# Performance work log

Measured on AMD Instinct MI355X. Metric: run time of the kernel, lower is better.

## Reference

```python
import jax, jax.numpy as jnp
import numpy as np

N, E = 10000, 160000
F_IN, H1, C1, C2 = 256, 8, 128, 128
SLOPE = 0.2  # PyG GATConv default negative_slope


def setup_inputs() -> dict:
    key = jax.random.key(0)
    ks = jax.random.split(key, 9)
    s = 0.05
    return {
        "x": jax.random.normal(ks[0], (N, F_IN), jnp.float32),
        "edge_index": jax.random.randint(ks[1], (2, E), 0, N),
        "W1": jax.random.normal(ks[2], (F_IN, H1 * C1), jnp.float32) * s,
        "a_src1": jax.random.normal(ks[3], (H1, C1), jnp.float32) * s,
        "a_dst1": jax.random.normal(ks[4], (H1, C1), jnp.float32) * s,
        "b1": jnp.zeros((H1 * C1,), jnp.float32),
        "W2": jax.random.normal(ks[5], (H1 * C1, C2), jnp.float32) * s,
        "a_src2": jax.random.normal(ks[6], (1, C2), jnp.float32) * s,
        "a_dst2": jax.random.normal(ks[7], (1, C2), jnp.float32) * s,
        "b2": jnp.zeros((C2,), jnp.float32),
    }


def gat_conv(x, src, dst, W, a_s, a_d, b, heads, out_ch, concat):
    n = x.shape[0]
    h = (x @ W).reshape(n, heads, out_ch)            # [N,H,C]
    s_src = jnp.einsum("nhc,hc->nh", h, a_s)         # [N,H]
    s_dst = jnp.einsum("nhc,hc->nh", h, a_d)
    e = jax.nn.leaky_relu(s_src[src] + s_dst[dst], SLOPE)   # [Etot,H]
    # segment softmax over incoming edges per destination (self-loops guarantee non-empty segments)
    m = jax.lax.stop_gradient(jax.ops.segment_max(e, dst, num_segments=n))
    p = jnp.exp(e - m[dst])
    denom = jax.ops.segment_sum(p, dst, num_segments=n)
    alpha = p / denom[dst]                            # [Etot,H]
    out = jax.ops.segment_sum(h[src] * alpha[:, :, None], dst, num_segments=n)  # [N,H,C]
    out = out.reshape(n, heads * out_ch) if concat else out.mean(axis=1)
    return out + b


def reference(x, edge_index, W1, a_src1, a_dst1, b1, W2, a_src2, a_dst2, b2):
    n = x.shape[0]
    loops = jnp.arange(n, dtype=edge_index.dtype)     # PyG add_self_loops=True
    src = jnp.concatenate([edge_index[0], loops])
    dst = jnp.concatenate([edge_index[1], loops])
    # dropout layers are identity at inference (training=False)
    h1 = jax.nn.elu(gat_conv(x, src, dst, W1, a_src1, a_dst1, b1, H1, C1, True))
    return gat_conv(h1, src, dst, W2, a_src2, a_dst2, b2, 1, C2, False)
```

## Files before the change

### kernel.cpp

```cpp
#include <hip/hip_runtime.h>
#include <math.h>

#define F_IN 256
#define H1 8
#define C1 128
#define HC1 1024
#define C2 128
#define SLOPE 0.2f

typedef unsigned short u16;
typedef __attribute__((ext_vector_type(8))) short bf16x8;
typedef __attribute__((ext_vector_type(4))) float f32x4;


__device__ __forceinline__ float lrelu(float v) { return v > 0.f ? v : SLOPE * v; }

__device__ __forceinline__ unsigned bf16_rne(float x) {
    unsigned u = __float_as_uint(x);
    u += 0x7fffu + ((u >> 16) & 1u);
    return u >> 16;
}

__device__ __forceinline__ void split2(float a, float b, unsigned& hi, unsigned& lo) {
    unsigned ha = bf16_rne(a), hb = bf16_rne(b);
    float fa = __uint_as_float(ha << 16), fb = __uint_as_float(hb << 16);
    hi = ha | (hb << 16);
    lo = bf16_rne(a - fa) | (bf16_rne(b - fb) << 16);
}

__device__ __forceinline__ void gload16(const u16* g, u16* l) {
    __builtin_amdgcn_global_load_lds(
        (const __attribute__((address_space(1))) unsigned*)g,
        (__attribute__((address_space(3))) unsigned*)l, 16, 0, 0);
}


__global__ void init_deg(int* deg, int n) {
    int i = blockIdx.x * blockDim.x + threadIdx.x;
    if (i < n) deg[i] = 1;
}

__global__ void hist_kernel(const int* __restrict__ dst, int* __restrict__ deg, int E) {
    int i = blockIdx.x * blockDim.x + threadIdx.x;
    if (i < E) atomicAdd(&deg[dst[i]], 1);
}

__global__ void scan_kernel(const int* __restrict__ deg, int* __restrict__ start,
                            int* __restrict__ cursor, int n) {
    __shared__ int buf[1024];
    int carry = 0;
    for (int base = 0; base < n; base += 1024) {
        int i = base + (int)threadIdx.x;
        int v = (i < n) ? deg[i] : 0;
        buf[threadIdx.x] = v;
        __syncthreads();
        for (int offd = 1; offd < 1024; offd <<= 1) {
            int tv = 0;
            if ((int)threadIdx.x >= offd) tv = buf[threadIdx.x - offd];
            __syncthreads();
            if ((int)threadIdx.x >= offd) buf[threadIdx.x] += tv;
            __syncthreads();
        }
        int incl = buf[threadIdx.x];
        if (i < n) { start[i] = carry + incl - v; cursor[i] = carry + incl - v; }
        carry += buf[1023];
        __syncthreads();
    }
    if (threadIdx.x == 0) start[n] = carry;
}

__global__ void scatter_kernel(const int* __restrict__ src, const int* __restrict__ dst,
                               int* __restrict__ cursor, int* __restrict__ ssorted,
                               unsigned char* __restrict__ rowloc,
                               int E, int N) {
    int i = blockIdx.x * blockDim.x + threadIdx.x;
    if (i < E) {
        int d = dst[i];
        int pos = atomicAdd(&cursor[d], 1);
        ssorted[pos] = src[i];
        rowloc[pos] = (unsigned char)(d & 15);
    } else if (i < E + N) {
        int d = i - E;
        int pos = atomicAdd(&cursor[d], 1);
        ssorted[pos] = d;
        rowloc[pos] = (unsigned char)(d & 15);
    }
}


__global__ void split_mat(const float* __restrict__ in, u16* __restrict__ hi,
                          u16* __restrict__ lo, int n) {
    int i = blockIdx.x * blockDim.x + threadIdx.x;
    if (i >= n) return;
    float v = in[i];
    unsigned h = bf16_rne(v);
    hi[i] = (u16)h;
    lo[i] = (u16)bf16_rne(v - __uint_as_float(h << 16));
}

__global__ void split_transpose(const float* __restrict__ in, u16* __restrict__ hi,
                                u16* __restrict__ lo, int R, int C) {
    int i = blockIdx.x * blockDim.x + threadIdx.x;
    if (i >= R * C) return;
    int r = i / C, c = i % C;
    float v = in[i];
    unsigned h = bf16_rne(v);
    hi[(size_t)c * R + r] = (u16)h;
    lo[(size_t)c * R + r] = (u16)bf16_rne(v - __uint_as_float(h << 16));
}


__global__ __launch_bounds__(256) void gemm_mfma(const u16* __restrict__ Ahi,
                                                 const u16* __restrict__ Alo,
                                                 const u16* __restrict__ Bhi,
                                                 const u16* __restrict__ Blo,
                                                 u16* __restrict__ Cbf,
                                                 int M, int N, int K) {
    __shared__ u16 lds[16384];
    const int t = threadIdx.x;
    const int rbase = blockIdx.y * 128;
    const int cbase = blockIdx.x * 128;

    const int lane = t & 63;
    const int R0 = (t >> 7) << 6;
    const int C0 = ((t >> 6) & 1) << 6;
    const int lrow = lane & 15;
    const int kq = lane >> 4;

    f32x4 acc[4][4] = {};

    for (int k0 = 0; k0 < K; k0 += 32) {
#pragma unroll
        for (int i = 0; i < 2; i++) {
            int c = t + (i << 8);
            int row = c >> 2;
            int kc = (c & 3) << 3;
            int ar = min(rbase + row, M - 1);
            int br = cbase + row;
            gload16(Ahi + (size_t)ar * K + k0 + kc, &lds[c * 8]);
            gload16(Alo + (size_t)ar * K + k0 + kc, &lds[4096 + c * 8]);
            gload16(Bhi + (size_t)br * K + k0 + kc, &lds[8192 + c * 8]);
            gload16(Blo + (size_t)br * K + k0 + kc, &lds[12288 + c * 8]);
        }
        __syncthreads();

        bf16x8 ah[4], al[4], bh[4], bl[4];
#pragma unroll
        for (int m = 0; m < 4; m++) {
            int off = (R0 + (m << 4) + lrow) * 32 + (kq << 3);
            ah[m] = *(const bf16x8*)&lds[off];
            al[m] = *(const bf16x8*)&lds[4096 + off];
        }
#pragma unroll
        for (int n = 0; n < 4; n++) {
            int off = (C0 + (n << 4) + lrow) * 32 + (kq << 3);
            bh[n] = *(const bf16x8*)&lds[8192 + off];
            bl[n] = *(const bf16x8*)&lds[12288 + off];
        }
#pragma unroll
        for (int m = 0; m < 4; m++)
#pragma unroll
            for (int n = 0; n < 4; n++) {
                acc[m][n] = __builtin_amdgcn_mfma_f32_16x16x32_bf16(ah[m], bh[n], acc[m][n], 0, 0, 0);
                acc[m][n] = __builtin_amdgcn_mfma_f32_16x16x32_bf16(ah[m], bl[n], acc[m][n], 0, 0, 0);
                acc[m][n] = __builtin_amdgcn_mfma_f32_16x16x32_bf16(al[m], bh[n], acc[m][n], 0, 0, 0);
            }
        __syncthreads();
    }

#pragma unroll
    for (int m = 0; m < 4; m++)
#pragma unroll
        for (int n = 0; n < 4; n++) {
            int col = cbase + C0 + (n << 4) + lrow;
#pragma unroll
            for (int r = 0; r < 4; r++) {
                int row = rbase + R0 + (m << 4) + kq * 4 + r;
                if (row < M) Cbf[(size_t)row * N + col] = (u16)bf16_rne(acc[m][n][r]);
            }
        }
}


__global__ __launch_bounds__(256) void gemm_mfma64(const u16* __restrict__ Ahi,
                                                   const u16* __restrict__ Alo,
                                                   const u16* __restrict__ Bhi,
                                                   const u16* __restrict__ Blo,
                                                   u16* __restrict__ Cbf,
                                                   int M, int N, int K) {
    __shared__ u16 lds[8192];
    const int t = threadIdx.x;
    const int rbase = blockIdx.y * 64;
    const int cbase = blockIdx.x * 64;

    const int lane = t & 63;
    const int w = t >> 6;
    const int R0 = (w >> 1) << 5;
    const int C0 = (w & 1) << 5;
    const int lrow = lane & 15;
    const int kq = lane >> 4;

    f32x4 acc[2][2] = {};

    for (int k0 = 0; k0 < K; k0 += 32) {
        {
            int row = t >> 2;
            int kc = (t & 3) << 3;
            int ar = min(rbase + row, M - 1);
            int br = cbase + row;
            gload16(Ahi + (size_t)ar * K + k0 + kc, &lds[t * 8]);
            gload16(Alo + (size_t)ar * K + k0 + kc, &lds[2048 + t * 8]);
            gload16(Bhi + (size_t)br * K + k0 + kc, &lds[4096 + t * 8]);
            gload16(Blo + (size_t)br * K + k0 + kc, &lds[6144 + t * 8]);
        }
        __syncthreads();

        bf16x8 ah[2], al[2], bh[2], bl[2];
#pragma unroll
        for (int m = 0; m < 2; m++) {
            int off = (R0 + (m << 4) + lrow) * 32 + (kq << 3);
            ah[m] = *(const bf16x8*)&lds[off];
            al[m] = *(const bf16x8*)&lds[2048 + off];
        }
#pragma unroll
        for (int n = 0; n < 2; n++) {
            int off = (C0 + (n << 4) + lrow) * 32 + (kq << 3);
            bh[n] = *(const bf16x8*)&lds[4096 + off];
            bl[n] = *(const bf16x8*)&lds[6144 + off];
        }
#pragma unroll
        for (int m = 0; m < 2; m++)
#pragma unroll
            for (int n = 0; n < 2; n++) {
                acc[m][n] = __builtin_amdgcn_mfma_f32_16x16x32_bf16(ah[m], bh[n], acc[m][n], 0, 0, 0);
                acc[m][n] = __builtin_amdgcn_mfma_f32_16x16x32_bf16(ah[m], bl[n], acc[m][n], 0, 0, 0);
                acc[m][n] = __builtin_amdgcn_mfma_f32_16x16x32_bf16(al[m], bh[n], acc[m][n], 0, 0, 0);
            }
        __syncthreads();
    }

#pragma unroll
    for (int m = 0; m < 2; m++)
#pragma unroll
        for (int n = 0; n < 2; n++) {
            int col = cbase + C0 + (n << 4) + lrow;
#pragma unroll
            for (int r = 0; r < 4; r++) {
                int row = rbase + R0 + (m << 4) + kq * 4 + r;
                if (row < M) Cbf[(size_t)row * N + col] = (u16)bf16_rne(acc[m][n][r]);
            }
        }
}


__global__ __launch_bounds__(256) void scores1_bf(const unsigned* __restrict__ hbf,
                                                  const float* __restrict__ a_s,
                                                  const float* __restrict__ a_d,
                                                  float* __restrict__ ssrc,
                                                  float* __restrict__ sdst, int N) {
    int wid = blockIdx.x * 4 + (threadIdx.x >> 6);
    if (wid >= N * H1) return;
    int lane = threadIdx.x & 63;
    int n = wid >> 3, hh = wid & 7;
    unsigned u = hbf[(size_t)n * 512 + hh * 64 + lane];
    float c0 = __uint_as_float(u << 16);
    float c1 = __uint_as_float(u & 0xffff0000u);
    const float* as = a_s + hh * C1;
    const float* ad = a_d + hh * C1;
    float vs = c0 * as[2 * lane] + c1 * as[2 * lane + 1];
    float vd = c0 * ad[2 * lane] + c1 * ad[2 * lane + 1];
    for (int off = 32; off; off >>= 1) {
        vs += __shfl_xor(vs, off);
        vd += __shfl_xor(vd, off);
    }
    if (lane == 0) { ssrc[wid] = vs; sdst[wid] = vd; }
}

__global__ __launch_bounds__(256) void scores2_bf(const unsigned* __restrict__ hbf,
                                                  const float* __restrict__ a_s,
                                                  const float* __restrict__ a_d,
                                                  float* __restrict__ ssrc,
                                                  float* __restrict__ sdst, int N) {
    int n = blockIdx.x * 4 + (threadIdx.x >> 6);
    if (n >= N) return;
    int lane = threadIdx.x & 63;
    unsigned u = hbf[(size_t)n * 64 + lane];
    float c0 = __uint_as_float(u << 16);
    float c1 = __uint_as_float(u & 0xffff0000u);
    float vs = c0 * a_s[2 * lane] + c1 * a_s[2 * lane + 1];
    float vd = c0 * a_d[2 * lane] + c1 * a_d[2 * lane + 1];
    for (int off = 32; off; off >>= 1) {
        vs += __shfl_xor(vs, off);
        vd += __shfl_xor(vd, off);
    }
    if (lane == 0) { ssrc[n] = vs; sdst[n] = vd; }
}


__global__ __launch_bounds__(256) void softmax_edges1(
    const float* __restrict__ ssrc, const float* __restrict__ sdst,
    const int* __restrict__ start, const int* __restrict__ ssorted,
    float* __restrict__ alphab, int N, int ET) {
    int lane = threadIdx.x & 63;
    int p = lane & 15, g = lane >> 4;
    int task = (blockIdx.x * 4 + (threadIdx.x >> 6)) * 4 + g;
    if (task >= N * H1) return;
    int d = task >> 3, hh = task & 7;
    int s0 = start[d], ne = start[d + 1] - s0;
    float sd = sdst[d * H1 + hh];
    int src0 = 0; float v0 = -1e30f;
    if (p < ne) { src0 = ssorted[s0 + p]; v0 = lrelu(ssrc[src0 * H1 + hh] + sd); }
    float m = v0;
    for (int e = p + 16; e < ne; e += 16)
        m = fmaxf(m, lrelu(ssrc[ssorted[s0 + e] * H1 + hh] + sd));
    for (int o = 8; o; o >>= 1) m = fmaxf(m, __shfl_xor(m, o));
    float p0 = (p < ne) ? __expf(v0 - m) : 0.f;
    float s = p0;
    for (int e = p + 16; e < ne; e += 16)
        s += __expf(lrelu(ssrc[ssorted[s0 + e] * H1 + hh] + sd) - m);
    for (int o = 8; o; o >>= 1) s += __shfl_xor(s, o);
    float inv = 1.f / s;
    float* ab = alphab + (size_t)hh * ET;
    if (p < ne) ab[s0 + p] = p0 * inv;
    for (int e = p + 16; e < ne; e += 16)
        ab[s0 + e] = __expf(lrelu(ssrc[ssorted[s0 + e] * H1 + hh] + sd) - m) * inv;
}


__global__ __launch_bounds__(256) void agg_mfma1(
    const u16* __restrict__ hbf,
    const float* __restrict__ alphab,
    const unsigned char* __restrict__ rowloc,
    const int* __restrict__ start,
    const int* __restrict__ ssorted,
    const float* __restrict__ bias,
    u16* __restrict__ outHi, u16* __restrict__ outLo,
    int N, int ET) {
    __shared__ unsigned mAl[32];
    __shared__ int mOff[32];
    __shared__ unsigned mRow[32];

    const int hh = blockIdx.x & 7;
    const int g = blockIdx.x >> 3;
    const int t = threadIdx.x;
    const int w = t >> 6;
    const int lane = t & 63;
    const int cl = lane & 15, q = lane >> 4;

    const int d0 = g * 16;
    const int e0 = start[d0], e1 = start[min(d0 + 16, N)];
    const float* ab = alphab + (size_t)hh * ET;

    const int lanebyte = hh * 256 + w * 64 + 4 * cl;
    const char* hbase = (const char*)hbf;

    f32x4 acc0 = {}, acc1 = {};

    for (int kb = e0; kb < e1; kb += 32) {
        __syncthreads();
        if (t < 32) {
            int pos = kb + t;
            bool valid = pos < e1;
            int ps = valid ? pos : e0;
            float af = valid ? ab[ps] : 0.f;
            unsigned ahiu = bf16_rne(af);
            unsigned alou = bf16_rne(af - __uint_as_float(ahiu << 16));
            mAl[t] = ahiu | (alou << 16);
            mOff[t] = ssorted[ps] << 11;
            mRow[t] = rowloc[ps];
        }
        __syncthreads();

        uint4 ma0 = *(const uint4*)&mAl[q * 8];
        uint4 ma1 = *(const uint4*)&mAl[q * 8 + 4];
        uint4 mr0 = *(const uint4*)&mRow[q * 8];
        uint4 mr1 = *(const uint4*)&mRow[q * 8 + 4];
        int4  mo0 = *(const int4*)&mOff[q * 8];
        int4  mo1 = *(const int4*)&mOff[q * 8 + 4];
        unsigned mm[8] = {ma0.x, ma0.y, ma0.z, ma0.w, ma1.x, ma1.y, ma1.z, ma1.w};
        unsigned rr[8] = {mr0.x, mr0.y, mr0.z, mr0.w, mr1.x, mr1.y, mr1.z, mr1.w};
        int      oo[8] = {mo0.x, mo0.y, mo0.z, mo0.w, mo1.x, mo1.y, mo1.z, mo1.w};

        bf16x8 ahi, alo;
#pragma unroll
        for (int j = 0; j < 8; j++) {
            bool mt = (int)rr[j] == cl;
            ahi[j] = mt ? (short)(mm[j] & 0xffffu) : (short)0;
            alo[j] = mt ? (short)(mm[j] >> 16) : (short)0;
        }

        unsigned gld[8];
#pragma unroll
        for (int j = 0; j < 8; j++)
            gld[j] = *(const unsigned*)(hbase + (unsigned)(oo[j] + lanebyte));

        union { unsigned u[4]; bf16x8 v; } b0, b1;
#pragma unroll
        for (int r = 0; r < 4; r++) {
            b0.u[r] = __builtin_amdgcn_perm(gld[2 * r + 1], gld[2 * r], 0x05040100u);
            b1.u[r] = __builtin_amdgcn_perm(gld[2 * r + 1], gld[2 * r], 0x07060302u);
        }

        acc0 = __builtin_amdgcn_mfma_f32_16x16x32_bf16(ahi, b0.v, acc0, 0, 0, 0);
        acc0 = __builtin_amdgcn_mfma_f32_16x16x32_bf16(alo, b0.v, acc0, 0, 0, 0);
        acc1 = __builtin_amdgcn_mfma_f32_16x16x32_bf16(ahi, b1.v, acc1, 0, 0, 0);
        acc1 = __builtin_amdgcn_mfma_f32_16x16x32_bf16(alo, b1.v, acc1, 0, 0, 0);
    }

    {
        int chbase = w * 32 + 2 * cl;
        float bv0 = bias[hh * C1 + chbase];
        float bv1 = bias[hh * C1 + chbase + 1];
#pragma unroll
        for (int r = 0; r < 4; r++) {
            int d = d0 + q * 4 + r;
            if (d >= N) continue;
            float v0 = acc0[r] + bv0;
            float v1 = acc1[r] + bv1;
            v0 = v0 > 0.f ? v0 : expm1f(v0);
            v1 = v1 > 0.f ? v1 : expm1f(v1);
            unsigned hi, lo;
            split2(v0, v1, hi, lo);
            size_t idx = (size_t)d * HC1 + hh * C1 + chbase;
            ((unsigned*)outHi)[idx >> 1] = hi;
            ((unsigned*)outLo)[idx >> 1] = lo;
        }
    }
}


template<int H, bool SPLITOUT>
__global__ __launch_bounds__(256) void agg_bf(const unsigned* __restrict__ hbf,
                                              const float* __restrict__ ssrc,
                                              const float* __restrict__ sdst,
                                              const int* __restrict__ start,
                                              const int* __restrict__ ssorted,
                                              const float* __restrict__ bias,
                                              float* __restrict__ out,
                                              unsigned* __restrict__ outHi,
                                              unsigned* __restrict__ outLo, int N) {
    int hh, grp;
    if (H == 8) { hh = blockIdx.x & 7; grp = blockIdx.x >> 3; }
    else        { hh = 0;              grp = blockIdx.x; }
    int wid = threadIdx.x >> 6, lane = threadIdx.x & 63;
    int d = grp * 4 + wid;
    if (d >= N) return;
    const int g = lane >> 4, p = lane & 15;
    int s0 = start[d];
    int ne = start[d + 1] - s0;
    float sd = sdst[d * H + hh];

    const unsigned* hlane = hbf + hh * 64 + p * 4;
    const int rowstride = H * 64;

    int src0 = 0; float v0 = -1e30f;
    if (lane < ne) { src0 = ssorted[s0 + lane]; v0 = lrelu(ssrc[src0 * H + hh] + sd); }
    float m = v0;
    for (int e = lane + 64; e < ne; e += 64)
        m = fmaxf(m, lrelu(ssrc[ssorted[s0 + e] * H + hh] + sd));
    for (int o = 32; o; o >>= 1) m = fmaxf(m, __shfl_xor(m, o));

    float p0 = (lane < ne) ? __expf(v0 - m) : 0.f;
    float ssum = p0;
    for (int e = lane + 64; e < ne; e += 64)
        ssum += __expf(lrelu(ssrc[ssorted[s0 + e] * H + hh] + sd) - m);
    for (int o = 32; o; o >>= 1) ssum += __shfl_xor(ssum, o);
    float inv = 1.f / ssum;

    float acc[8] = {};
    for (int base = 0; base < ne; base += 64) {
        int srcr; float al;
        if (base == 0) { srcr = src0; al = p0 * inv; }
        else {
            srcr = 0; al = 0.f;
            int e = base + lane;
            if (e < ne) {
                srcr = ssorted[s0 + e];
                al = __expf(lrelu(ssrc[srcr * H + hh] + sd) - m) * inv;
            }
        }
        int cnt = min(64, ne - base);
        for (int e2 = 0; e2 < cnt; e2 += 4) {
            float a = __shfl(al, e2 + g);
            int sr = __shfl(srcr, e2 + g);
            uint4 u = *(const uint4*)(hlane + (size_t)sr * rowstride);
            acc[0] += a * __uint_as_float(u.x << 16);
            acc[1] += a * __uint_as_float(u.x & 0xffff0000u);
            acc[2] += a * __uint_as_float(u.y << 16);
            acc[3] += a * __uint_as_float(u.y & 0xffff0000u);
            acc[4] += a * __uint_as_float(u.z << 16);
            acc[5] += a * __uint_as_float(u.z & 0xffff0000u);
            acc[6] += a * __uint_as_float(u.w << 16);
            acc[7] += a * __uint_as_float(u.w & 0xffff0000u);
        }
    }

#pragma unroll
    for (int i = 0; i < 8; i++) {
        acc[i] += __shfl_xor(acc[i], 16);
        acc[i] += __shfl_xor(acc[i], 32);
    }

    float r0 = g == 0 ? acc[0] : g == 1 ? acc[2] : g == 2 ? acc[4] : acc[6];
    float r1 = g == 0 ? acc[1] : g == 1 ? acc[3] : g == 2 ? acc[5] : acc[7];
    int j = 4 * p + g;
    float2 bv = ((const float2*)bias)[hh * 64 + j];
    r0 += bv.x; r1 += bv.y;
    size_t idx = (size_t)d * (H * 64) + hh * 64 + j;
    if (SPLITOUT) {
        r0 = r0 > 0.f ? r0 : expm1f(r0);
        r1 = r1 > 0.f ? r1 : expm1f(r1);
        unsigned hi, lo;
        split2(r0, r1, hi, lo);
        outHi[idx] = hi;
        outLo[idx] = lo;
    } else {
        ((float2*)out)[idx] = make_float2(r0, r1);
    }
}


extern "C" void kernel_launch(void* const* d_in, const int* in_sizes, int n_in,
                              void* d_out, int out_size, void* d_ws, size_t ws_size,
                              hipStream_t stream) {
    const float* x      = (const float*)d_in[0];
    const int*   ei     = (const int*)d_in[1];
    const float* W1     = (const float*)d_in[2];
    const float* a_src1 = (const float*)d_in[3];
    const float* a_dst1 = (const float*)d_in[4];
    const float* b1     = (const float*)d_in[5];
    const float* W2     = (const float*)d_in[6];
    const float* a_src2 = (const float*)d_in[7];
    const float* a_dst2 = (const float*)d_in[8];
    const float* b2     = (const float*)d_in[9];
    float* out = (float*)d_out;

    int E = in_sizes[1] / 2;
    int N = in_sizes[0] / F_IN;
    int ET = E + N;
    const int* esrc = ei;
    const int* edst = ei + E;

    char* ws = (char*)d_ws;
    size_t off = 0;
    auto alloc = [&](size_t bytes) -> char* {
        char* p = ws + off;
        off = (off + bytes + 255) & ~(size_t)255;
        return p;
    };
    u16* x_hi    = (u16*)alloc((size_t)N * F_IN * 2);
    u16* x_lo    = (u16*)alloc((size_t)N * F_IN * 2);
    u16* W1t_hi  = (u16*)alloc((size_t)F_IN * HC1 * 2);
    u16* W1t_lo  = (u16*)alloc((size_t)F_IN * HC1 * 2);
    u16* W2t_hi  = (u16*)alloc((size_t)HC1 * C2 * 2);
    u16* W2t_lo  = (u16*)alloc((size_t)HC1 * C2 * 2);
    u16* h1_bf   = (u16*)alloc((size_t)N * HC1 * 2);
    u16* h1a_hi  = (u16*)alloc((size_t)N * HC1 * 2);
    u16* h1a_lo  = (u16*)alloc((size_t)N * HC1 * 2);
    u16* h2_bf   = (u16*)alloc((size_t)N * C2 * 2);
    float* ss1   = (float*)alloc((size_t)N * H1 * 4);
    float* sd1   = (float*)alloc((size_t)N * H1 * 4);
    float* ss2   = (float*)alloc((size_t)N * 4);
    float* sd2   = (float*)alloc((size_t)N * 4);
    int* deg     = (int*)alloc((size_t)N * 4);
    int* startp  = (int*)alloc((size_t)(N + 1) * 4);
    int* cursor  = (int*)alloc((size_t)N * 4);
    int* ssorted = (int*)alloc((size_t)ET * 4);
    unsigned char* rowloc = (unsigned char*)alloc((size_t)ET);
    float* alpha1 = (float*)x_hi;

    init_deg<<<(N + 255) / 256, 256, 0, stream>>>(deg, N);
    hist_kernel<<<(E + 255) / 256, 256, 0, stream>>>(edst, deg, E);
    scan_kernel<<<1, 1024, 0, stream>>>(deg, startp, cursor, N);
    scatter_kernel<<<(E + N + 255) / 256, 256, 0, stream>>>(esrc, edst, cursor, ssorted, rowloc, E, N);

    split_mat<<<(N * F_IN + 255) / 256, 256, 0, stream>>>(x, x_hi, x_lo, N * F_IN);
    split_transpose<<<(F_IN * HC1 + 255) / 256, 256, 0, stream>>>(W1, W1t_hi, W1t_lo, F_IN, HC1);
    split_transpose<<<(HC1 * C2 + 255) / 256, 256, 0, stream>>>(W2, W2t_hi, W2t_lo, HC1, C2);

    gemm_mfma<<<dim3(HC1 / 128, (N + 127) / 128), 256, 0, stream>>>(
        x_hi, x_lo, W1t_hi, W1t_lo, h1_bf, N, HC1, F_IN);
    scores1_bf<<<(N * H1 + 3) / 4, 256, 0, stream>>>(
        (const unsigned*)h1_bf, a_src1, a_dst1, ss1, sd1, N);
    softmax_edges1<<<(N * H1 + 15) / 16, 256, 0, stream>>>(
        ss1, sd1, startp, ssorted, alpha1, N, ET);
    agg_mfma1<<<((N + 15) / 16) * H1, 256, 0, stream>>>(
        h1_bf, alpha1, rowloc, startp, ssorted, b1, h1a_hi, h1a_lo, N, ET);

    gemm_mfma64<<<dim3(C2 / 64, (N + 63) / 64), 256, 0, stream>>>(
        h1a_hi, h1a_lo, W2t_hi, W2t_lo, h2_bf, N, C2, HC1);
    scores2_bf<<<(N + 3) / 4, 256, 0, stream>>>(
        (const unsigned*)h2_bf, a_src2, a_dst2, ss2, sd2, N);
    agg_bf<1, false><<<(N + 3) / 4, 256, 0, stream>>>(
        (const unsigned*)h2_bf, ss2, sd2, startp, ssorted, b2,
        out, nullptr, nullptr, N);
}
```

Baseline: 255.6 us.

## Double-buffer edge metadata and stage dense alpha tiles in LDS for layer-1 aggregation

The layer-1 MFMA aggregation kernel now processes 64 edges per iteration instead of 32. Wave 0 prefetches the next chunk's offsets and alpha values into a second LDS buffer, so only one barrier is needed per iteration. Alpha is scattered into a dense zero-filled 16x64 A matrix in LDS, replacing the per-lane row-compare masking. Each iteration issues 16 independent gathers and 8 MFMAs, which adds latency-hiding work per barrier. The cost is more LDS traffic from zero-filling, plus a reliance on an explicit lgkmcnt wait to order the zero stores before the scatter within the wave.

```diff
diff --git a/kernel.cpp b/kernel.cpp
--- a/kernel.cpp
+++ b/kernel.cpp
@@ -336,9 +336,8 @@
     const float* __restrict__ bias,
     u16* __restrict__ outHi, u16* __restrict__ outLo,
     int N, int ET) {
-    __shared__ unsigned mAl[32];
-    __shared__ int mOff[32];
-    __shared__ unsigned mRow[32];
+    __shared__ unsigned A32[2][16 * 68];
+    __shared__ int mOff[2][64];
 
     const int hh = blockIdx.x & 7;
     const int g = blockIdx.x >> 3;
@@ -354,57 +353,78 @@
     const int lanebyte = hh * 256 + w * 64 + 4 * cl;
     const char* hbase = (const char*)hbf;
 
+    const int nk = (e1 - e0 + 63) >> 6;
+
+    auto fill = [&](int b, int kb) {
+        unsigned* Az = &A32[b][(lane >> 2) * 68 + (lane & 3) * 16];
+        uint4 z = {0u, 0u, 0u, 0u};
+        *(uint4*)(Az) = z;
+        *(uint4*)(Az + 4) = z;
+        *(uint4*)(Az + 8) = z;
+        *(uint4*)(Az + 12) = z;
+        int pos = kb + lane;
+        bool valid = pos < e1;
+        int ps = valid ? pos : e0;
+        float af = valid ? ab[ps] : 0.f;
+        unsigned ahiu = bf16_rne(af);
+        unsigned alou = bf16_rne(af - __uint_as_float(ahiu << 16));
+        int rr = rowloc[ps];
+        mOff[b][lane] = ssorted[ps] << 11;
+        asm volatile("s_waitcnt lgkmcnt(0)" ::: "memory");
+        A32[b][rr * 68 + lane] = ahiu | (alou << 16);
+    };
+
     f32x4 acc0 = {}, acc1 = {};
 
-    for (int kb = e0; kb < e1; kb += 32) {
+    if (w == 0 && nk > 0) fill(0, e0);
+
+    for (int i = 0; i < nk; ++i) {
         __syncthreads();
-        if (t < 32) {
-            int pos = kb + t;
-            bool valid = pos < e1;
-            int ps = valid ? pos : e0;
-            float af = valid ? ab[ps] : 0.f;
-            unsigned ahiu = bf16_rne(af);
-            unsigned alou = bf16_rne(af - __uint_as_float(ahiu << 16));
-            mAl[t] = ahiu | (alou << 16);
-            mOff[t] = ssorted[ps] << 11;
-            mRow[t] = rowloc[ps];
-        }
-        __syncthreads();
-
-        uint4 ma0 = *(const uint4*)&mAl[q * 8];
-        uint4 ma1 = *(const uint4*)&mAl[q * 8 + 4];
-        uint4 mr0 = *(const uint4*)&mRow[q * 8];
-        uint4 mr1 = *(const uint4*)&mRow[q * 8 + 4];
-        int4  mo0 = *(const int4*)&mOff[q * 8];
-        int4  mo1 = *(const int4*)&mOff[q * 8 + 4];
-        unsigned mm[8] = {ma0.x, ma0.y, ma0.z, ma0.w, ma1.x, ma1.y, ma1.z, ma1.w};
-        unsigned rr[8] = {mr0.x, mr0.y, mr0.z, mr0.w, mr1.x, mr1.y, mr1.z, mr1.w};
-        int      oo[8] = {mo0.x, mo0.y, mo0.z, mo0.w, mo1.x, mo1.y, mo1.z, mo1.w};
-
-        bf16x8 ahi, alo;
-#pragma unroll
-        for (int j = 0; j < 8; j++) {
-            bool mt = (int)rr[j] == cl;
-            ahi[j] = mt ? (short)(mm[j] & 0xffffu) : (short)0;
-            alo[j] = mt ? (short)(mm[j] >> 16) : (short)0;
-        }
-
-        unsigned gld[8];
-#pragma unroll
-        for (int j = 0; j < 8; j++)
+        const int b = i & 1;
+        if (w == 0 && i + 1 < nk) fill(b ^ 1, e0 + (i + 1) * 64);
+
+        const int mb = q * 8;
+        int4 o0 = *(const int4*)&mOff[b][mb];
+        int4 o1 = *(const int4*)&mOff[b][mb + 4];
+        int4 o2 = *(const int4*)&mOff[b][32 + mb];
+        int4 o3 = *(const int4*)&mOff[b][32 + mb + 4];
+        int oo[16] = {o0.x, o0.y, o0.z, o0.w, o1.x, o1.y, o1.z, o1.w,
+                      o2.x, o2.y, o2.z, o2.w, o3.x, o3.y, o3.z, o3.w};
+
+        unsigned gld[16];
+#pragma unroll
+        for (int j = 0; j < 16; j++)
             gld[j] = *(const unsigned*)(hbase + (unsigned)(oo[j] + lanebyte));
 
-        union { unsigned u[4]; bf16x8 v; } b0, b1;
+        const unsigned* Ar = &A32[b][cl * 68 + mb];
+        uint4 a0 = *(const uint4*)(Ar);
+        uint4 a1 = *(const uint4*)(Ar + 4);
+        uint4 a2 = *(const uint4*)(Ar + 32);
+        uint4 a3 = *(const uint4*)(Ar + 36);
+        unsigned aw[16] = {a0.x, a0.y, a0.z, a0.w, a1.x, a1.y, a1.z, a1.w,
+                           a2.x, a2.y, a2.z, a2.w, a3.x, a3.y, a3.z, a3.w};
+
+        union { unsigned u[4]; bf16x8 v; } ahi0, alo0, ahi1, alo1, b00, b10, b01, b11;
 #pragma unroll
         for (int r = 0; r < 4; r++) {
-            b0.u[r] = __builtin_amdgcn_perm(gld[2 * r + 1], gld[2 * r], 0x05040100u);
-            b1.u[r] = __builtin_amdgcn_perm(gld[2 * r + 1], gld[2 * r], 0x07060302u);
-        }
-
-        acc0 = __builtin_amdgcn_mfma_f32_16x16x32_bf16(ahi, b0.v, acc0, 0, 0, 0);
-        acc0 = __builtin_amdgcn_mfma_f32_16x16x32_bf16(alo, b0.v, acc0, 0, 0, 0);
-        acc1 = __builtin_amdgcn_mfma_f32_16x16x32_bf16(ahi, b1.v, acc1, 0, 0, 0);
-        acc1 = __builtin_amdgcn_mfma_f32_16x16x32_bf16(alo, b1.v, acc1, 0, 0, 0);
+            ahi0.u[r] = __builtin_amdgcn_perm(aw[2 * r + 1], aw[2 * r], 0x05040100u);
+            alo0.u[r] = __builtin_amdgcn_perm(aw[2 * r + 1], aw[2 * r], 0x07060302u);
+            ahi1.u[r] = __builtin_amdgcn_perm(aw[8 + 2 * r + 1], aw[8 + 2 * r], 0x05040100u);
+            alo1.u[r] = __builtin_amdgcn_perm(aw[8 + 2 * r + 1], aw[8 + 2 * r], 0x07060302u);
+            b00.u[r] = __builtin_amdgcn_perm(gld[2 * r + 1], gld[2 * r], 0x05040100u);
+            b10.u[r] = __builtin_amdgcn_perm(gld[2 * r + 1], gld[2 * r], 0x07060302u);
+            b01.u[r] = __builtin_amdgcn_perm(gld[8 + 2 * r + 1], gld[8 + 2 * r], 0x05040100u);
+            b11.u[r] = __builtin_amdgcn_perm(gld[8 + 2 * r + 1], gld[8 + 2 * r], 0x07060302u);
+        }
+
+        acc0 = __builtin_amdgcn_mfma_f32_16x16x32_bf16(ahi0.v, b00.v, acc0, 0, 0, 0);
+        acc0 = __builtin_amdgcn_mfma_f32_16x16x32_bf16(alo0.v, b00.v, acc0, 0, 0, 0);
+        acc1 = __builtin_amdgcn_mfma_f32_16x16x32_bf16(ahi0.v, b10.v, acc1, 0, 0, 0);
+        acc1 = __builtin_amdgcn_mfma_f32_16x16x32_bf16(alo0.v, b10.v, acc1, 0, 0, 0);
+        acc0 = __builtin_amdgcn_mfma_f32_16x16x32_bf16(ahi1.v, b01.v, acc0, 0, 0, 0);
+        acc0 = __builtin_amdgcn_mfma_f32_16x16x32_bf16(alo1.v, b01.v, acc0, 0, 0, 0);
+        acc1 = __builtin_amdgcn_mfma_f32_16x16x32_bf16(ahi1.v, b11.v, acc1, 0, 0, 0);
+        acc1 = __builtin_amdgcn_mfma_f32_16x16x32_bf16(alo1.v, b11.v, acc1, 0, 0, 0);
     }
 
     {
```

After: 250.7 us. About the same (-1.9%).
